# Kernel optimization log

Hardware: AMD Instinct MI355X
Metric: run time of the kernel (lower is better)

Reference implementation:

```python
import jax, jax.numpy as jnp
import numpy as np

B, N, E, H = 8, 16, 256, 256
EPS = 1e-5


def _ln(x, g, b):
    m = jnp.mean(x, axis=-1, keepdims=True)
    v = jnp.mean(jnp.square(x - m), axis=-1, keepdims=True)
    return (x - m) * jax.lax.rsqrt(v + EPS) * g + b


def setup_inputs() -> dict:
    key = jax.random.key(0)
    ks = jax.random.split(key, 24)
    s = 0.05
    inp = {
        "source_entities": jax.random.normal(ks[0], (B, N, E), jnp.float32),
        "source_relations": jax.random.uniform(ks[1], (B, N, N), jnp.float32),
        "target_entities": jax.random.normal(ks[2], (B, N, E), jnp.float32),
        "target_relations": jax.random.uniform(ks[3], (B, N, N), jnp.float32),
        # relation_encoder: Linear(2E->H), LayerNorm(H), ReLU, Linear(H->H)
        "rel_W1": jax.random.normal(ks[4], (2 * E, H), jnp.float32) * s,
        "rel_b1": jnp.zeros((H,), jnp.float32),
        "rel_g1": jnp.ones((H,), jnp.float32),
        "rel_be1": jnp.zeros((H,), jnp.float32),
        "rel_W2": jax.random.normal(ks[5], (H, H), jnp.float32) * s,
        "rel_b2": jnp.zeros((H,), jnp.float32),
        # mapping_network: Linear(2H->H), LayerNorm(H), ReLU, Linear(H->1)
        "map_W1": jax.random.normal(ks[6], (2 * H, H), jnp.float32) * s,
        "map_b1": jnp.zeros((H,), jnp.float32),
        "map_g": jnp.ones((H,), jnp.float32),
        "map_be": jnp.zeros((H,), jnp.float32),
        "map_W2": jax.random.normal(ks[7], (H, 1), jnp.float32) * s,
        "map_b2": jnp.zeros((1,), jnp.float32),
        # correspondence_scorer: Linear(2E->H), ReLU, Linear(H->1)
        "cor_W1": jax.random.normal(ks[8], (2 * E, H), jnp.float32) * s,
        "cor_b1": jnp.zeros((H,), jnp.float32),
        "cor_W2": jax.random.normal(ks[9], (H, 1), jnp.float32) * s,
        "cor_b2": jnp.zeros((1,), jnp.float32),
    }
    return inp


def _encode_relations(ent, rel, W1, b1, g1, be1, W2, b2):
    # ent: [B,N,E]; rel: [B,N,N].  Equivalent to cat([e_i, e_j]) @ W1 by
    # splitting W1 into the rows multiplying e_i and e_j (avoids concat).
    Wi, Wj = W1[:E], W1[E:]
    h = (jnp.einsum("bie,eh->bih", ent, Wi)[:, :, None, :]
         + jnp.einsum("bje,eh->bjh", ent, Wj)[:, None, :, :] + b1)  # [B,N,N,H]
    h = jax.nn.relu(_ln(h, g1, be1))
    h = jnp.einsum("bijh,hk->bijk", h, W2) + b2
    mask = (rel > 0).astype(h.dtype)[..., None]
    h = h * mask  # zeros where no relation, matching scatter into zeros tensor
    return h.reshape(ent.shape[0], N * N, H)


def _pairwise_score(a, b, W1, b1, W2, b2, g=None, be=None):
    # score over all (i,j) pairs: cat([a_i, b_j]) -> MLP -> scalar
    d = a.shape[-1]
    Wa, Wb = W1[:d], W1[d:]
    h = (jnp.einsum("bsd,dh->bsh", a, Wa)[:, :, None, :]
         + jnp.einsum("btd,dh->bth", b, Wb)[:, None, :, :] + b1)  # [B,S,T,H]
    if g is not None:
        h = _ln(h, g, be)
    h = jax.nn.relu(h)
    return (jnp.einsum("bsth,ho->bsto", h, W2) + b2)[..., 0]  # [B,S,T]


def reference(source_entities, source_relations, target_entities, target_relations,
              rel_W1, rel_b1, rel_g1, rel_be1, rel_W2, rel_b2,
              map_W1, map_b1, map_g, map_be, map_W2, map_b2,
              cor_W1, cor_b1, cor_W2, cor_b2):
    src_rel = _encode_relations(source_entities, source_relations,
                                rel_W1, rel_b1, rel_g1, rel_be1, rel_W2, rel_b2)
    tgt_rel = _encode_relations(target_entities, target_relations,
                                rel_W1, rel_b1, rel_g1, rel_be1, rel_W2, rel_b2)
    mapping_scores = _pairwise_score(src_rel, tgt_rel, map_W1, map_b1,
                                     map_W2, map_b2, map_g, map_be)
    corr_scores = _pairwise_score(source_entities, target_entities,
                                  cor_W1, cor_b1, cor_W2, cor_b2)
    mapping_scores = jax.nn.softmax(mapping_scores, axis=-1)
    corr_scores = jax.nn.softmax(corr_scores, axis=-1)
    return mapping_scores, corr_scores
```

## Files before the change

### kernel.cpp

```cpp
#include <hip/hip_runtime.h>

#define EDIM 256
#define HDIM 256

typedef float v2f __attribute__((ext_vector_type(2)));
__device__ __forceinline__ v2f splat2(float x) { v2f r; r.x = x; r.y = x; return r; }
__device__ __forceinline__ v2f mk2(float a, float b) { v2f r; r.x = a; r.y = b; return r; }
__device__ __forceinline__ v2f pkfma(v2f a, v2f b, v2f c) { return __builtin_elementwise_fma(a, b, c); }

__device__ __forceinline__ float waveAllSum(float v) {
  #pragma unroll
  for (int m = 32; m >= 1; m >>= 1) v += __shfl_xor(v, m, 64);
  return v;
}

__global__ __launch_bounds__(256) void k_proj(
    const float* __restrict__ srcE, const float* __restrict__ tgtE,
    const float* __restrict__ relW1, const float* __restrict__ relb1,
    const float* __restrict__ corW1, const float* __restrict__ corb1,
    float* __restrict__ Ps, float* __restrict__ Qs,
    float* __restrict__ Pt, float* __restrict__ Qt,
    float* __restrict__ CA, float* __restrict__ CB)
{
  const int which = blockIdx.y;
  const int row0  = blockIdx.x * 8;
  const int h     = threadIdx.x;

  const float* A; const float* W; const float* bias; float* out;
  if (which == 0)      { A = srcE; W = relW1;              bias = relb1;   out = Ps; }
  else if (which == 1) { A = srcE; W = relW1 + EDIM*HDIM;  bias = nullptr; out = Qs; }
  else if (which == 2) { A = tgtE; W = relW1;              bias = relb1;   out = Pt; }
  else if (which == 3) { A = tgtE; W = relW1 + EDIM*HDIM;  bias = nullptr; out = Qt; }
  else if (which == 4) { A = srcE; W = corW1;              bias = nullptr; out = CA; }
  else                 { A = tgtE; W = corW1 + EDIM*HDIM;  bias = corb1;   out = CB; }

  __shared__ float arow[8][EDIM];
  #pragma unroll
  for (int r = 0; r < 8; ++r) arow[r][h] = A[(row0 + r)*EDIM + h];
  __syncthreads();

  float acc[8];
  const float init = bias ? bias[h] : 0.0f;
  #pragma unroll
  for (int r = 0; r < 8; ++r) acc[r] = init;

  for (int d = 0; d < EDIM; d += 4) {
    const float w0 = W[(d+0)*HDIM + h];
    const float w1 = W[(d+1)*HDIM + h];
    const float w2 = W[(d+2)*HDIM + h];
    const float w3 = W[(d+3)*HDIM + h];
    #pragma unroll
    for (int r = 0; r < 8; ++r) {
      const float4 av = *(const float4*)&arow[r][d];
      acc[r] = fmaf(av.x,w0, fmaf(av.y,w1, fmaf(av.z,w2, fmaf(av.w,w3, acc[r]))));
    }
  }
  #pragma unroll
  for (int r = 0; r < 8; ++r) out[(row0 + r)*HDIM + h] = acc[r];
}

__global__ __launch_bounds__(256) void k_encode(
    const float* __restrict__ Ps, const float* __restrict__ Qs,
    const float* __restrict__ relS,
    const float* __restrict__ Pt, const float* __restrict__ Qt,
    const float* __restrict__ relT,
    const float* __restrict__ g1, const float* __restrict__ be1,
    const float* __restrict__ W2, const float* __restrict__ b2,
    const float* __restrict__ mapW1, const float* __restrict__ mapb1,
    const float* __restrict__ mapg, const float* __restrict__ mapbe,
    const float* __restrict__ mapW2,
    float2* __restrict__ SAp, float* __restrict__ SAr, float* __restrict__ TB,
    float* __restrict__ rsS, float* __restrict__ qsS,
    float* __restrict__ rsT, float* __restrict__ qsT,
    float4* __restrict__ gbw)
{
  const int side = blockIdx.y;
  const float* P   = side ? Pt   : Ps;
  const float* Q   = side ? Qt   : Qs;
  const float* rel = side ? relT : relS;

  const int row0 = blockIdx.x * 4;
  const int b   = row0 >> 8;
  const int ij0 = row0 & 255;
  const int i   = ij0 >> 4;
  const int j0  = ij0 & 15;
  const int h    = threadIdx.x;
  const int wave = threadIdx.x >> 6;
  const int lane = threadIdx.x & 63;

  if (side == 0 && blockIdx.x == 0)
    gbw[h] = make_float4(mapg[h], mapbe[h], mapW2[h], 0.0f);

  __shared__ v2f rlp[2][HDIM];
  __shared__ float red[4][8];

  const float pv = P[(b*16 + i)*HDIM + h];
  float x[4];
  #pragma unroll
  for (int r = 0; r < 4; ++r) x[r] = pv + Q[(b*16 + j0 + r)*HDIM + h];

  {
    float s1[4], s2[4];
    #pragma unroll
    for (int r = 0; r < 4; ++r) { s1[r] = x[r]; s2[r] = x[r]*x[r]; }
    #pragma unroll
    for (int m = 32; m >= 1; m >>= 1) {
      #pragma unroll
      for (int r = 0; r < 4; ++r) {
        s1[r] += __shfl_xor(s1[r], m, 64);
        s2[r] += __shfl_xor(s2[r], m, 64);
      }
    }
    if (lane == 0) {
      #pragma unroll
      for (int r = 0; r < 4; ++r) { red[wave][2*r] = s1[r]; red[wave][2*r+1] = s2[r]; }
    }
  }
  __syncthreads();

  {
    const float gh = g1[h], beh = be1[h];
    float val[4];
    #pragma unroll
    for (int r = 0; r < 4; ++r) {
      const float S1 = red[0][2*r] + red[1][2*r] + red[2][2*r] + red[3][2*r];
      const float S2 = red[0][2*r+1] + red[1][2*r+1] + red[2][2*r+1] + red[3][2*r+1];
      const float mean = S1 * (1.0f/256.0f);
      const float var  = S2 * (1.0f/256.0f) - mean*mean;
      const float rinv = rsqrtf(var + 1e-5f);
      val[r] = fmaxf(fmaf((x[r] - mean)*rinv, gh, beh), 0.0f);
    }
    rlp[0][h] = mk2(val[0], val[1]);
    rlp[1][h] = mk2(val[2], val[3]);
  }
  __syncthreads();

  v2f a01 = {0.f,0.f}, a23 = {0.f,0.f};
  #pragma unroll 2
  for (int k = 0; k < HDIM; k += 4) {
    const float w0 = W2[(k+0)*HDIM + h];
    const float w1 = W2[(k+1)*HDIM + h];
    const float w2 = W2[(k+2)*HDIM + h];
    const float w3 = W2[(k+3)*HDIM + h];
    const float4 p01a = *(const float4*)&rlp[0][k];
    const float4 p01b = *(const float4*)&rlp[0][k+2];
    const float4 p23a = *(const float4*)&rlp[1][k];
    const float4 p23b = *(const float4*)&rlp[1][k+2];
    a01 = pkfma(mk2(p01a.x,p01a.y), splat2(w0), a01);
    a01 = pkfma(mk2(p01a.z,p01a.w), splat2(w1), a01);
    a01 = pkfma(mk2(p01b.x,p01b.y), splat2(w2), a01);
    a01 = pkfma(mk2(p01b.z,p01b.w), splat2(w3), a01);
    a23 = pkfma(mk2(p23a.x,p23a.y), splat2(w0), a23);
    a23 = pkfma(mk2(p23a.z,p23a.w), splat2(w1), a23);
    a23 = pkfma(mk2(p23b.x,p23b.y), splat2(w2), a23);
    a23 = pkfma(mk2(p23b.z,p23b.w), splat2(w3), a23);
  }
  __syncthreads();

  {
    const float* relRow = rel + (b*16 + i)*16;
    const float bb = b2[h];
    const v2f m01 = mk2(relRow[j0+0] > 0.f ? 1.f : 0.f, relRow[j0+1] > 0.f ? 1.f : 0.f);
    const v2f m23 = mk2(relRow[j0+2] > 0.f ? 1.f : 0.f, relRow[j0+3] > 0.f ? 1.f : 0.f);
    rlp[0][h] = (a01 + splat2(bb)) * m01;
    rlp[1][h] = (a23 + splat2(bb)) * m23;
  }
  __syncthreads();

  const float* Wm = side ? (mapW1 + EDIM*HDIM) : mapW1;
  v2f c01 = {0.f,0.f}, c23 = {0.f,0.f};
  #pragma unroll 2
  for (int k = 0; k < HDIM; k += 4) {
    const float w0 = Wm[(k+0)*HDIM + h];
    const float w1 = Wm[(k+1)*HDIM + h];
    const float w2 = Wm[(k+2)*HDIM + h];
    const float w3 = Wm[(k+3)*HDIM + h];
    const float4 p01a = *(const float4*)&rlp[0][k];
    const float4 p01b = *(const float4*)&rlp[0][k+2];
    const float4 p23a = *(const float4*)&rlp[1][k];
    const float4 p23b = *(const float4*)&rlp[1][k+2];
    c01 = pkfma(mk2(p01a.x,p01a.y), splat2(w0), c01);
    c01 = pkfma(mk2(p01a.z,p01a.w), splat2(w1), c01);
    c01 = pkfma(mk2(p01b.x,p01b.y), splat2(w2), c01);
    c01 = pkfma(mk2(p01b.z,p01b.w), splat2(w3), c01);
    c23 = pkfma(mk2(p23a.x,p23a.y), splat2(w0), c23);
    c23 = pkfma(mk2(p23a.z,p23a.w), splat2(w1), c23);
    c23 = pkfma(mk2(p23b.x,p23b.y), splat2(w2), c23);
    c23 = pkfma(mk2(p23b.z,p23b.w), splat2(w3), c23);
  }
  {
    const float init2 = side ? mapb1[h] : 0.0f;
    c01 = c01 + splat2(init2);
    c23 = c23 + splat2(init2);
  }

  {
    float s1[4] = {c01.x, c01.y, c23.x, c23.y};
    float s2[4] = {c01.x*c01.x, c01.y*c01.y, c23.x*c23.x, c23.y*c23.y};
    #pragma unroll
    for (int m = 32; m >= 1; m >>= 1) {
      #pragma unroll
      for (int r = 0; r < 4; ++r) {
        s1[r] += __shfl_xor(s1[r], m, 64);
        s2[r] += __shfl_xor(s2[r], m, 64);
      }
    }
    __syncthreads();
    if (lane == 0) {
      #pragma unroll
      for (int r = 0; r < 4; ++r) { red[wave][2*r] = s1[r]; red[wave][2*r+1] = s2[r]; }
    }
  }
  __syncthreads();
  if (threadIdx.x < 8) {
    const float v = red[0][threadIdx.x] + red[1][threadIdx.x] +
                    red[2][threadIdx.x] + red[3][threadIdx.x];
    const int r = threadIdx.x >> 1;
    float* rs = side ? rsT : rsS;
    float* qs = side ? qsT : qsS;
    if (threadIdx.x & 1) qs[row0 + r] = v; else rs[row0 + r] = v;
  }

  if (side == 0) {
    const int spBase = b*128 + (ij0 >> 1);
    SAp[(spBase + 0)*HDIM + h] = make_float2(c01.x, c01.y);
    SAp[(spBase + 1)*HDIM + h] = make_float2(c23.x, c23.y);
    SAr[(row0 + 0)*HDIM + h] = c01.x;
    SAr[(row0 + 1)*HDIM + h] = c01.y;
    SAr[(row0 + 2)*HDIM + h] = c23.x;
    SAr[(row0 + 3)*HDIM + h] = c23.y;
  } else {
    TB[(row0 + 0)*HDIM + h] = c01.x;
    TB[(row0 + 1)*HDIM + h] = c01.y;
    TB[(row0 + 2)*HDIM + h] = c23.x;
    TB[(row0 + 3)*HDIM + h] = c23.y;
  }
}

__global__ __launch_bounds__(256) void k_cross(
    const float* __restrict__ SAr, const float* __restrict__ TB,
    float* __restrict__ G)
{
  const int b  = blockIdx.z;
  const int s0 = blockIdx.y * 32;
  const int t0 = blockIdx.x * 32;
  const int tx = threadIdx.x & 15;
  const int ty = threadIdx.x >> 4;

  const float* SAb = SAr + ((b<<8) + s0)*HDIM;
  const float* TBb = TB  + ((b<<8) + t0)*HDIM;

  __shared__ float As[32][68], Bs[32][68];
  float acc00 = 0.f, acc01 = 0.f, acc10 = 0.f, acc11 = 0.f;

  const int lr = threadIdx.x >> 3;
  const int lc = (threadIdx.x & 7) * 8;

  for (int kk = 0; kk < HDIM; kk += 64) {
    *(float4*)&As[lr][lc]   = *(const float4*)&SAb[lr*HDIM + kk + lc];
    *(float4*)&As[lr][lc+4] = *(const float4*)&SAb[lr*HDIM + kk + lc + 4];
    *(float4*)&Bs[lr][lc]   = *(const float4*)&TBb[lr*HDIM + kk + lc];
    *(float4*)&Bs[lr][lc+4] = *(const float4*)&TBb[lr*HDIM + kk + lc + 4];
    __syncthreads();
    #pragma unroll
    for (int k = 0; k < 64; k += 4) {
      const float4 a0 = *(const float4*)&As[tx][k];
      const float4 a1 = *(const float4*)&As[tx+16][k];
      const float4 b0 = *(const float4*)&Bs[ty][k];
      const float4 b1 = *(const float4*)&Bs[ty+16][k];
      acc00 = fmaf(a0.x,b0.x, fmaf(a0.y,b0.y, fmaf(a0.z,b0.z, fmaf(a0.w,b0.w, acc00))));
      acc01 = fmaf(a0.x,b1.x, fmaf(a0.y,b1.y, fmaf(a0.z,b1.z, fmaf(a0.w,b1.w, acc01))));
      acc10 = fmaf(a1.x,b0.x, fmaf(a1.y,b0.y, fmaf(a1.z,b0.z, fmaf(a1.w,b0.w, acc10))));
      acc11 = fmaf(a1.x,b1.x, fmaf(a1.y,b1.y, fmaf(a1.z,b1.z, fmaf(a1.w,b1.w, acc11))));
    }
    __syncthreads();
  }

  float* Gb = G + (((b<<8) + t0)<<8) + s0;
  Gb[(ty   )*256 + tx     ] = acc00;
  Gb[(ty   )*256 + tx + 16] = acc10;
  Gb[(ty+16)*256 + tx     ] = acc01;
  Gb[(ty+16)*256 + tx + 16] = acc11;
}

__global__ __launch_bounds__(256) void k_scores(
    const float2* __restrict__ SApf, const float* __restrict__ TB,
    const float* __restrict__ G,
    const float* __restrict__ rsS, const float* __restrict__ qsS,
    const float* __restrict__ rsT, const float* __restrict__ qsT,
    const float4* __restrict__ gbw,
    const float* __restrict__ CA, const float* __restrict__ CB,
    const float* __restrict__ cW2,
    float* __restrict__ mapOut, float* __restrict__ corOut)
{
  const int wave = threadIdx.x >> 6;
  const int lane = threadIdx.x & 63;

  if (blockIdx.x >= 512) {
    const int bs = (blockIdx.x - 512)*4 + wave;
    const int b  = bs >> 4;
    const float4 ca4 = *(const float4*)(CA + bs*HDIM + lane*4);
    const float4 w24 = *(const float4*)(cW2 + lane*4);
    float sc[16];
    #pragma unroll
    for (int t = 0; t < 16; ++t) {
      const float4 cb4 = *(const float4*)(CB + (b*16 + t)*HDIM + lane*4);
      float p = fmaxf(ca4.x + cb4.x, 0.0f)*w24.x
              + fmaxf(ca4.y + cb4.y, 0.0f)*w24.y
              + fmaxf(ca4.z + cb4.z, 0.0f)*w24.z
              + fmaxf(ca4.w + cb4.w, 0.0f)*w24.w;
      sc[t] = waveAllSum(p);
    }
    float mx = sc[0];
    #pragma unroll
    for (int t = 1; t < 16; ++t) mx = fmaxf(mx, sc[t]);
    float se = 0.0f;
    #pragma unroll
    for (int t = 0; t < 16; ++t) { sc[t] = __expf(sc[t] - mx); se += sc[t]; }
    if (lane < 16) corOut[bs*16 + lane] = sc[lane] / se;
    return;
  }

  const int b  = blockIdx.x >> 6;
  const int s0 = (blockIdx.x & 63) * 4;
  const int t  = (wave << 6) + lane;

  const float* tbrow = TB + ((b<<8) + t)*HDIM;
  const v2f* sp0 = (const v2f*)SApf + ((b<<7) + (s0>>1))*HDIM;
  const v2f* sp1 = sp0 + HDIM;

  v2f al01, bt01, al23, bt23;
  {
    const float4 gv = *(const float4*)&G[(((b<<8) + t)<<8) + s0];
    const float rt = rsT[(b<<8) + t];
    const float qt = qsT[(b<<8) + t];
    const float Gv[4] = {gv.x, gv.y, gv.z, gv.w};
    float alv[4], btv[4];
    #pragma unroll
    for (int si = 0; si < 4; ++si) {
      const float mean = (rsS[(b<<8) + s0 + si] + rt) * (1.0f/256.0f);
      const float e2   = (qsS[(b<<8) + s0 + si] + qt + 2.0f*Gv[si]) * (1.0f/256.0f);
      const float rinv = rsqrtf(e2 - mean*mean + 1e-5f);
      alv[si] = rinv;
      btv[si] = -mean * rinv;
    }
    al01 = mk2(alv[0], alv[1]); bt01 = mk2(btv[0], btv[1]);
    al23 = mk2(alv[2], alv[3]); bt23 = mk2(btv[2], btv[3]);
  }

  v2f acc01 = {0.f,0.f}, acc23 = {0.f,0.f};
  const v2f zero = {0.f,0.f};
  #pragma unroll 2
  for (int h = 0; h < HDIM; h += 4) {
    const float4 tb4 = *(const float4*)&tbrow[h];
    const v2f a0 = sp0[h], a1 = sp0[h+1], a2 = sp0[h+2], a3 = sp0[h+3];
    const v2f c0 = sp1[h], c1 = sp1[h+1], c2 = sp1[h+2], c3 = sp1[h+3];
    const float4 q0 = gbw[h], q1 = gbw[h+1], q2 = gbw[h+2], q3 = gbw[h+3];
    v2f u, r;
    u = pkfma(a0 + splat2(tb4.x), al01, bt01);
    r = __builtin_elementwise_max(pkfma(u, splat2(q0.x), splat2(q0.y)), zero);
    acc01 = pkfma(r, splat2(q0.z), acc01);
    u = pkfma(c0 + splat2(tb4.x), al23, bt23);
    r = __builtin_elementwise_max(pkfma(u, splat2(q0.x), splat2(q0.y)), zero);
    acc23 = pkfma(r, splat2(q0.z), acc23);

    u = pkfma(a1 + splat2(tb4.y), al01, bt01);
    r = __builtin_elementwise_max(pkfma(u, splat2(q1.x), splat2(q1.y)), zero);
    acc01 = pkfma(r, splat2(q1.z), acc01);
    u = pkfma(c1 + splat2(tb4.y), al23, bt23);
    r = __builtin_elementwise_max(pkfma(u, splat2(q1.x), splat2(q1.y)), zero);
    acc23 = pkfma(r, splat2(q1.z), acc23);

    u = pkfma(a2 + splat2(tb4.z), al01, bt01);
    r = __builtin_elementwise_max(pkfma(u, splat2(q2.x), splat2(q2.y)), zero);
    acc01 = pkfma(r, splat2(q2.z), acc01);
    u = pkfma(c2 + splat2(tb4.z), al23, bt23);
    r = __builtin_elementwise_max(pkfma(u, splat2(q2.x), splat2(q2.y)), zero);
    acc23 = pkfma(r, splat2(q2.z), acc23);

    u = pkfma(a3 + splat2(tb4.w), al01, bt01);
    r = __builtin_elementwise_max(pkfma(u, splat2(q3.x), splat2(q3.y)), zero);
    acc01 = pkfma(r, splat2(q3.z), acc01);
    u = pkfma(c3 + splat2(tb4.w), al23, bt23);
    r = __builtin_elementwise_max(pkfma(u, splat2(q3.x), splat2(q3.y)), zero);
    acc23 = pkfma(r, splat2(q3.z), acc23);
  }

  __shared__ float sc[4][256];
  sc[0][t] = acc01.x; sc[1][t] = acc01.y; sc[2][t] = acc23.x; sc[3][t] = acc23.y;
  __syncthreads();

  float v0 = sc[wave][lane];
  float v1 = sc[wave][lane + 64];
  float v2 = sc[wave][lane + 128];
  float v3 = sc[wave][lane + 192];
  float mx = fmaxf(fmaxf(v0, v1), fmaxf(v2, v3));
  #pragma unroll
  for (int m = 32; m >= 1; m >>= 1) mx = fmaxf(mx, __shfl_xor(mx, m, 64));
  const float e0 = __expf(v0 - mx), e1 = __expf(v1 - mx);
  const float e2 = __expf(v2 - mx), e3 = __expf(v3 - mx);
  const float se = waveAllSum(e0 + e1 + e2 + e3);
  const float inv = 1.0f / se;
  float* orow = mapOut + ((b<<8) + s0 + wave)*256;
  orow[lane]       = e0 * inv;
  orow[lane + 64]  = e1 * inv;
  orow[lane + 128] = e2 * inv;
  orow[lane + 192] = e3 * inv;
}

extern "C" void kernel_launch(void* const* d_in, const int* in_sizes, int n_in,
                              void* d_out, int out_size, void* d_ws, size_t ws_size,
                              hipStream_t stream) {
  const float* srcE  = (const float*)d_in[0];
  const float* srcR  = (const float*)d_in[1];
  const float* tgtE  = (const float*)d_in[2];
  const float* tgtR  = (const float*)d_in[3];
  const float* relW1 = (const float*)d_in[4];
  const float* relb1 = (const float*)d_in[5];
  const float* relg1 = (const float*)d_in[6];
  const float* relbe1= (const float*)d_in[7];
  const float* relW2 = (const float*)d_in[8];
  const float* relb2 = (const float*)d_in[9];
  const float* mapW1 = (const float*)d_in[10];
  const float* mapb1 = (const float*)d_in[11];
  const float* mapg  = (const float*)d_in[12];
  const float* mapbe = (const float*)d_in[13];
  const float* mapW2 = (const float*)d_in[14];
  const float* corW1 = (const float*)d_in[16];
  const float* corb1 = (const float*)d_in[17];
  const float* corW2 = (const float*)d_in[18];

  float* ws   = (float*)d_ws;
  float* Ps   = ws;
  float* Qs   = Ps   + 32768;
  float* Pt   = Qs   + 32768;
  float* Qt   = Pt   + 32768;
  float* CA   = Qt   + 32768;
  float* CB   = CA   + 32768;
  float2* SAp = (float2*)(CB + 32768);
  float* SAr  = (float*)(SAp + 262144);
  float* TB   = SAr + 524288;
  float* G    = TB  + 524288;
  float* rsS  = G + 524288;
  float* qsS  = rsS + 2048;
  float* rsT  = qsS + 2048;
  float* qsT  = rsT + 2048;
  float4* gbw = (float4*)(qsT + 2048);

  float* mapOut = (float*)d_out;
  float* corOut = mapOut + 524288;

  k_proj<<<dim3(16, 6), 256, 0, stream>>>(srcE, tgtE, relW1, relb1, corW1, corb1,
                                          Ps, Qs, Pt, Qt, CA, CB);
  k_encode<<<dim3(512, 2), 256, 0, stream>>>(Ps, Qs, srcR,
                                             Pt, Qt, tgtR,
                                             relg1, relbe1, relW2, relb2,
                                             mapW1, mapb1, mapg, mapbe, mapW2,
                                             SAp, SAr, TB, rsS, qsS, rsT, qsT, gbw);
  k_cross<<<dim3(8, 8, 8), 256, 0, stream>>>(SAr, TB, G);
  k_scores<<<544, 256, 0, stream>>>(SAp, TB, G, rsS, qsS, rsT, qsT, gbw,
                                    CA, CB, corW2, mapOut, corOut);
}
```

Before: 83.00 us.

## Fold relation W2 into mapping W1 to remove one GEMM per pair

Precomputes C = relW2 @ mapW1 halves and d = relb2 @ mapW1 halves in the projection kernel. The encode kernel can then skip the separate relW2 matmul and apply the relation mask after the fused product, since the mask is a per-row scalar and commutes with the linear map. The encode kernel also grows to 512 threads covering 8 rows per block. This removes one 256x256 matvec per relation row, at the cost of extra blocks in k_proj and a small change in rounding from the reassociated product.

```diff
diff --git a/kernel.cpp b/kernel.cpp
--- a/kernel.cpp
+++ b/kernel.cpp
@@ -18,25 +18,42 @@
     const float* __restrict__ srcE, const float* __restrict__ tgtE,
     const float* __restrict__ relW1, const float* __restrict__ relb1,
     const float* __restrict__ corW1, const float* __restrict__ corb1,
+    const float* __restrict__ relW2, const float* __restrict__ relb2,
+    const float* __restrict__ mapW1,
     float* __restrict__ Ps, float* __restrict__ Qs,
     float* __restrict__ Pt, float* __restrict__ Qt,
-    float* __restrict__ CA, float* __restrict__ CB)
+    float* __restrict__ CA, float* __restrict__ CB,
+    float* __restrict__ Ca, float* __restrict__ Cb,
+    float* __restrict__ da, float* __restrict__ db)
 {
   const int which = blockIdx.y;
-  const int row0  = blockIdx.x * 8;
+  const int xb    = blockIdx.x;
   const int h     = threadIdx.x;
-
-  const float* A; const float* W; const float* bias; float* out;
-  if (which == 0)      { A = srcE; W = relW1;              bias = relb1;   out = Ps; }
-  else if (which == 1) { A = srcE; W = relW1 + EDIM*HDIM;  bias = nullptr; out = Qs; }
-  else if (which == 2) { A = tgtE; W = relW1;              bias = relb1;   out = Pt; }
-  else if (which == 3) { A = tgtE; W = relW1 + EDIM*HDIM;  bias = nullptr; out = Qt; }
-  else if (which == 4) { A = srcE; W = corW1;              bias = nullptr; out = CA; }
-  else                 { A = tgtE; W = corW1 + EDIM*HDIM;  bias = corb1;   out = CB; }
+  if (which < 6 && xb >= 16) return;
+  const int row0  = xb * 8;
+
+  const float* A = nullptr; const float* W; const float* bias = nullptr;
+  float* out;
+  if (which == 0)      { A = srcE; W = relW1;              bias = relb1; out = Ps; }
+  else if (which == 1) { A = srcE; W = relW1 + EDIM*HDIM;  out = Qs; }
+  else if (which == 2) { A = tgtE; W = relW1;              bias = relb1; out = Pt; }
+  else if (which == 3) { A = tgtE; W = relW1 + EDIM*HDIM;  out = Qt; }
+  else if (which == 4) { A = srcE; W = corW1;              out = CA; }
+  else if (which == 5) { A = tgtE; W = corW1 + EDIM*HDIM;  bias = corb1; out = CB; }
+  else if (which == 6) { W = mapW1;                        out = Ca; }
+  else                 { W = mapW1 + EDIM*HDIM;            out = Cb; }
 
   __shared__ float arow[8][EDIM];
-  #pragma unroll
-  for (int r = 0; r < 8; ++r) arow[r][h] = A[(row0 + r)*EDIM + h];
+  if (which < 6) {
+    #pragma unroll
+    for (int r = 0; r < 8; ++r) arow[r][h] = A[(row0 + r)*EDIM + h];
+  } else if (xb < 32) {
+    #pragma unroll
+    for (int r = 0; r < 8; ++r) arow[r][h] = relW2[(row0 + r)*EDIM + h];
+  } else {
+    #pragma unroll
+    for (int r = 0; r < 8; ++r) arow[r][h] = relb2[h];
+  }
   __syncthreads();
 
   float acc[8];
@@ -55,18 +72,25 @@
       acc[r] = fmaf(av.x,w0, fmaf(av.y,w1, fmaf(av.z,w2, fmaf(av.w,w3, acc[r]))));
     }
   }
-  #pragma unroll
-  for (int r = 0; r < 8; ++r) out[(row0 + r)*HDIM + h] = acc[r];
-}
-
-__global__ __launch_bounds__(256) void k_encode(
+
+  if (which < 6 || xb < 32) {
+    #pragma unroll
+    for (int r = 0; r < 8; ++r) out[(row0 + r)*HDIM + h] = acc[r];
+  } else {
+    float* d = (which == 6) ? da : db;
+    d[h] = acc[0];
+  }
+}
+
+__global__ __launch_bounds__(512) void k_encode(
     const float* __restrict__ Ps, const float* __restrict__ Qs,
     const float* __restrict__ relS,
     const float* __restrict__ Pt, const float* __restrict__ Qt,
     const float* __restrict__ relT,
     const float* __restrict__ g1, const float* __restrict__ be1,
-    const float* __restrict__ W2, const float* __restrict__ b2,
-    const float* __restrict__ mapW1, const float* __restrict__ mapb1,
+    const float* __restrict__ Ca, const float* __restrict__ Cb,
+    const float* __restrict__ da, const float* __restrict__ db,
+    const float* __restrict__ mapb1,
     const float* __restrict__ mapg, const float* __restrict__ mapbe,
     const float* __restrict__ mapW2,
     float2* __restrict__ SAp, float* __restrict__ SAr, float* __restrict__ TB,
@@ -79,25 +103,27 @@
   const float* Q   = side ? Qt   : Qs;
   const float* rel = side ? relT : relS;
 
-  const int row0 = blockIdx.x * 4;
+  const int row0 = blockIdx.x * 8;
   const int b   = row0 >> 8;
   const int ij0 = row0 & 255;
   const int i   = ij0 >> 4;
   const int j0  = ij0 & 15;
-  const int h    = threadIdx.x;
-  const int wave = threadIdx.x >> 6;
-  const int lane = threadIdx.x & 63;
-
-  if (side == 0 && blockIdx.x == 0)
+  const int tid  = threadIdx.x;
+  const int h    = tid & 255;
+  const int rg   = tid >> 8;
+  const int wave = tid >> 6;
+  const int lane = tid & 63;
+
+  if (side == 0 && blockIdx.x == 0 && rg == 0)
     gbw[h] = make_float4(mapg[h], mapbe[h], mapW2[h], 0.0f);
 
-  __shared__ v2f rlp[2][HDIM];
-  __shared__ float red[4][8];
+  __shared__ v2f rlp[2][2][HDIM];
+  __shared__ float red[8][8];
 
   const float pv = P[(b*16 + i)*HDIM + h];
   float x[4];
   #pragma unroll
-  for (int r = 0; r < 4; ++r) x[r] = pv + Q[(b*16 + j0 + r)*HDIM + h];
+  for (int r = 0; r < 4; ++r) x[r] = pv + Q[(b*16 + j0 + rg*4 + r)*HDIM + h];
 
   {
     float s1[4], s2[4];
@@ -120,78 +146,59 @@
 
   {
     const float gh = g1[h], beh = be1[h];
+    const int wb = rg*4;
     float val[4];
     #pragma unroll
     for (int r = 0; r < 4; ++r) {
-      const float S1 = red[0][2*r] + red[1][2*r] + red[2][2*r] + red[3][2*r];
-      const float S2 = red[0][2*r+1] + red[1][2*r+1] + red[2][2*r+1] + red[3][2*r+1];
+      const float S1 = red[wb+0][2*r] + red[wb+1][2*r] + red[wb+2][2*r] + red[wb+3][2*r];
+      const float S2 = red[wb+0][2*r+1] + red[wb+1][2*r+1] + red[wb+2][2*r+1] + red[wb+3][2*r+1];
       const float mean = S1 * (1.0f/256.0f);
       const float var  = S2 * (1.0f/256.0f) - mean*mean;
       const float rinv = rsqrtf(var + 1e-5f);
       val[r] = fmaxf(fmaf((x[r] - mean)*rinv, gh, beh), 0.0f);
     }
-    rlp[0][h] = mk2(val[0], val[1]);
-    rlp[1][h] = mk2(val[2], val[3]);
+    rlp[rg][0][h] = mk2(val[0], val[1]);
+    rlp[rg][1][h] = mk2(val[2], val[3]);
   }
   __syncthreads();
 
-  v2f a01 = {0.f,0.f}, a23 = {0.f,0.f};
-  #pragma unroll 2
-  for (int k = 0; k < HDIM; k += 4) {
-    const float w0 = W2[(k+0)*HDIM + h];
-    const float w1 = W2[(k+1)*HDIM + h];
-    const float w2 = W2[(k+2)*HDIM + h];
-    const float w3 = W2[(k+3)*HDIM + h];
-    const float4 p01a = *(const float4*)&rlp[0][k];
-    const float4 p01b = *(const float4*)&rlp[0][k+2];
-    const float4 p23a = *(const float4*)&rlp[1][k];
-    const float4 p23b = *(const float4*)&rlp[1][k+2];
-    a01 = pkfma(mk2(p01a.x,p01a.y), splat2(w0), a01);
-    a01 = pkfma(mk2(p01a.z,p01a.w), splat2(w1), a01);
-    a01 = pkfma(mk2(p01b.x,p01b.y), splat2(w2), a01);
-    a01 = pkfma(mk2(p01b.z,p01b.w), splat2(w3), a01);
-    a23 = pkfma(mk2(p23a.x,p23a.y), splat2(w0), a23);
-    a23 = pkfma(mk2(p23a.z,p23a.w), splat2(w1), a23);
-    a23 = pkfma(mk2(p23b.x,p23b.y), splat2(w2), a23);
-    a23 = pkfma(mk2(p23b.z,p23b.w), splat2(w3), a23);
-  }
-  __syncthreads();
-
-  {
-    const float* relRow = rel + (b*16 + i)*16;
-    const float bb = b2[h];
-    const v2f m01 = mk2(relRow[j0+0] > 0.f ? 1.f : 0.f, relRow[j0+1] > 0.f ? 1.f : 0.f);
-    const v2f m23 = mk2(relRow[j0+2] > 0.f ? 1.f : 0.f, relRow[j0+3] > 0.f ? 1.f : 0.f);
-    rlp[0][h] = (a01 + splat2(bb)) * m01;
-    rlp[1][h] = (a23 + splat2(bb)) * m23;
-  }
-  __syncthreads();
-
-  const float* Wm = side ? (mapW1 + EDIM*HDIM) : mapW1;
+  const float* C = side ? Cb : Ca;
   v2f c01 = {0.f,0.f}, c23 = {0.f,0.f};
   #pragma unroll 2
   for (int k = 0; k < HDIM; k += 4) {
-    const float w0 = Wm[(k+0)*HDIM + h];
-    const float w1 = Wm[(k+1)*HDIM + h];
-    const float w2 = Wm[(k+2)*HDIM + h];
-    const float w3 = Wm[(k+3)*HDIM + h];
-    const float4 p01a = *(const float4*)&rlp[0][k];
-    const float4 p01b = *(const float4*)&rlp[0][k+2];
-    const float4 p23a = *(const float4*)&rlp[1][k];
-    const float4 p23b = *(const float4*)&rlp[1][k+2];
-    c01 = pkfma(mk2(p01a.x,p01a.y), splat2(w0), c01);
-    c01 = pkfma(mk2(p01a.z,p01a.w), splat2(w1), c01);
-    c01 = pkfma(mk2(p01b.x,p01b.y), splat2(w2), c01);
-    c01 = pkfma(mk2(p01b.z,p01b.w), splat2(w3), c01);
-    c23 = pkfma(mk2(p23a.x,p23a.y), splat2(w0), c23);
-    c23 = pkfma(mk2(p23a.z,p23a.w), splat2(w1), c23);
-    c23 = pkfma(mk2(p23b.x,p23b.y), splat2(w2), c23);
-    c23 = pkfma(mk2(p23b.z,p23b.w), splat2(w3), c23);
-  }
+    const float w0 = C[(k+0)*HDIM + h];
+    const float w1 = C[(k+1)*HDIM + h];
+    const float w2 = C[(k+2)*HDIM + h];
+    const float w3 = C[(k+3)*HDIM + h];
+    const float4 pa = *(const float4*)&rlp[rg][0][k];
+    const float4 pb = *(const float4*)&rlp[rg][0][k+2];
+    const float4 qa = *(const float4*)&rlp[rg][1][k];
+    const float4 qb = *(const float4*)&rlp[rg][1][k+2];
+    c01 = pkfma(mk2(pa.x,pa.y), splat2(w0), c01);
+    c01 = pkfma(mk2(pa.z,pa.w), splat2(w1), c01);
+    c01 = pkfma(mk2(pb.x,pb.y), splat2(w2), c01);
+    c01 = pkfma(mk2(pb.z,pb.w), splat2(w3), c01);
+    c23 = pkfma(mk2(qa.x,qa.y), splat2(w0), c23);
+    c23 = pkfma(mk2(qa.z,qa.w), splat2(w1), c23);
+    c23 = pkfma(mk2(qb.x,qb.y), splat2(w2), c23);
+    c23 = pkfma(mk2(qb.z,qb.w), splat2(w3), c23);
+  }
+
   {
-    const float init2 = side ? mapb1[h] : 0.0f;
-    c01 = c01 + splat2(init2);
-    c23 = c23 + splat2(init2);
+    const float dv = (side ? db : da)[h];
+    c01 = c01 + splat2(dv);
+    c23 = c23 + splat2(dv);
+    const float* relRow = rel + (b*16 + i)*16;
+    const int jb = j0 + rg*4;
+    const v2f m01 = mk2(relRow[jb+0] > 0.f ? 1.f : 0.f, relRow[jb+1] > 0.f ? 1.f : 0.f);
+    const v2f m23 = mk2(relRow[jb+2] > 0.f ? 1.f : 0.f, relRow[jb+3] > 0.f ? 1.f : 0.f);
+    c01 = c01 * m01;
+    c23 = c23 * m23;
+    if (side) {
+      const float mb = mapb1[h];
+      c01 = c01 + splat2(mb);
+      c23 = c23 + splat2(mb);
+    }
   }
 
   {
@@ -212,28 +219,30 @@
     }
   }
   __syncthreads();
-  if (threadIdx.x < 8) {
-    const float v = red[0][threadIdx.x] + red[1][threadIdx.x] +
-                    red[2][threadIdx.x] + red[3][threadIdx.x];
-    const int r = threadIdx.x >> 1;
+  if (tid < 16) {
+    const int rg2 = tid >> 3, idx = tid & 7, r = idx >> 1;
+    const int wb = rg2*4;
+    const float v = red[wb+0][idx] + red[wb+1][idx] + red[wb+2][idx] + red[wb+3][idx];
     float* rs = side ? rsT : rsS;
     float* qs = side ? qsT : qsS;
-    if (threadIdx.x & 1) qs[row0 + r] = v; else rs[row0 + r] = v;
-  }
-
+    const int row = row0 + rg2*4 + r;
+    if (idx & 1) qs[row] = v; else rs[row] = v;
+  }
+
+  const int rbase = row0 + rg*4;
   if (side == 0) {
-    const int spBase = b*128 + (ij0 >> 1);
+    const int spBase = b*128 + ((ij0 + rg*4) >> 1);
     SAp[(spBase + 0)*HDIM + h] = make_float2(c01.x, c01.y);
     SAp[(spBase + 1)*HDIM + h] = make_float2(c23.x, c23.y);
-    SAr[(row0 + 0)*HDIM + h] = c01.x;
-    SAr[(row0 + 1)*HDIM + h] = c01.y;
-    SAr[(row0 + 2)*HDIM + h] = c23.x;
-    SAr[(row0 + 3)*HDIM + h] = c23.y;
+    SAr[(rbase + 0)*HDIM + h] = c01.x;
+    SAr[(rbase + 1)*HDIM + h] = c01.y;
+    SAr[(rbase + 2)*HDIM + h] = c23.x;
+    SAr[(rbase + 3)*HDIM + h] = c23.y;
   } else {
-    TB[(row0 + 0)*HDIM + h] = c01.x;
-    TB[(row0 + 1)*HDIM + h] = c01.y;
-    TB[(row0 + 2)*HDIM + h] = c23.x;
-    TB[(row0 + 3)*HDIM + h] = c23.y;
+    TB[(rbase + 0)*HDIM + h] = c01.x;
+    TB[(rbase + 1)*HDIM + h] = c01.y;
+    TB[(rbase + 2)*HDIM + h] = c23.x;
+    TB[(rbase + 3)*HDIM + h] = c23.y;
   }
 }
 
@@ -446,16 +455,23 @@
   float* rsT  = qsS + 2048;
   float* qsT  = rsT + 2048;
   float4* gbw = (float4*)(qsT + 2048);
+  float* Ca   = (float*)gbw + 1024;
+  float* Cb   = Ca + 65536;
+  float* da   = Cb + 65536;
+  float* db   = da + 256;
 
   float* mapOut = (float*)d_out;
   float* corOut = mapOut + 524288;
 
-  k_proj<<<dim3(16, 6), 256, 0, stream>>>(srcE, tgtE, relW1, relb1, corW1, corb1,
-                                          Ps, Qs, Pt, Qt, CA, CB);
-  k_encode<<<dim3(512, 2), 256, 0, stream>>>(Ps, Qs, srcR,
+  k_proj<<<dim3(33, 8), 256, 0, stream>>>(srcE, tgtE, relW1, relb1, corW1, corb1,
+                                          relW2, relb2, mapW1,
+                                          Ps, Qs, Pt, Qt, CA, CB,
+                                          Ca, Cb, da, db);
+  k_encode<<<dim3(256, 2), 512, 0, stream>>>(Ps, Qs, srcR,
                                              Pt, Qt, tgtR,
-                                             relg1, relbe1, relW2, relb2,
-                                             mapW1, mapb1, mapg, mapbe, mapW2,
+                                             relg1, relbe1,
+                                             Ca, Cb, da, db,
+                                             mapb1, mapg, mapbe, mapW2,
                                              SAp, SAr, TB, rsS, qsS, rsT, qsT, gbw);
   k_cross<<<dim3(8, 8, 8), 256, 0, stream>>>(SAr, TB, G);
   k_scores<<<544, 256, 0, stream>>>(SAp, TB, G, rsS, qsS, rsT, qsT, gbw,
```

New measurement: 74.37 us. 10.4% less time.
